# Kernel optimization log

Measured on AMD Instinct MI355X. Metric: run time of the kernel, lower is better.

The kernel has to match this reference:

```python
import jax, jax.numpy as jnp
import numpy as np

B, NQ, NK = 4, 2048, 2048
DQ = DK = DV = 512
H = 8
DS = DV // H  # 64


def _layernorm(x, g, b, eps=1e-5):
    m = jnp.mean(x, axis=-1, keepdims=True)
    v = jnp.var(x, axis=-1, keepdims=True)
    return (x - m) * jax.lax.rsqrt(v + eps) * g + b


def setup_inputs() -> dict:
    key = jax.random.key(0)
    ks = jax.random.split(key, 16)
    def lin(k, fan_in, fan_out):
        # torch nn.Linear default init: U(-1/sqrt(fan_in), 1/sqrt(fan_in))
        bound = 1.0 / np.sqrt(fan_in)
        k1, k2 = jax.random.split(k)
        W = jax.random.uniform(k1, (fan_in, fan_out), jnp.float32, -bound, bound)
        b = jax.random.uniform(k2, (fan_out,), jnp.float32, -bound, bound)
        return W, b
    Wq, bq = lin(ks[0], DQ, DV)
    Wk, bk = lin(ks[1], DK, DV)
    Wv, bv = lin(ks[2], DK, DV)
    W0, b0 = lin(ks[3], DV, DV)
    W1, b1 = lin(ks[4], DV, DV)
    # xavier_uniform for kp/vp of shape (1, DS): bound = sqrt(6/(1+DS))
    xb = np.sqrt(6.0 / (1 + DS))
    kp = jax.random.uniform(ks[5], (DS,), jnp.float32, -xb, xb)
    vp = jax.random.uniform(ks[6], (DS,), jnp.float32, -xb, xb)
    return {
        "Q": jax.random.normal(ks[7], (B, NQ, DQ), jnp.float32),
        "K": jax.random.normal(ks[8], (B, NK, DK), jnp.float32),
        "Kpos": jax.random.uniform(ks[9], (B, NQ, NK), jnp.float32),
        "Wq": Wq, "bq": bq, "Wk": Wk, "bk": bk, "Wv": Wv, "bv": bv,
        "kp": kp, "vp": vp,
        "W0": W0, "b0": b0, "W1": W1, "b1": b1,
        "g0": jnp.ones((DV,), jnp.float32), "be0": jnp.zeros((DV,), jnp.float32),
        "g1": jnp.ones((DV,), jnp.float32), "be1": jnp.zeros((DV,), jnp.float32),
    }


def reference(Q, K, Kpos, Wq, bq, Wk, bk, Wv, bv, kp, vp, W0, b0, W1, b1, g0, be0, g1, be1):
    Qp = Q @ Wq + bq                       # [B,NQ,DV]
    Kp = K @ Wk + bk                       # [B,NK,DV]
    Vp = K @ Wv + bv                       # [B,NK,DV]
    # head split (torch split/cat along batch == reshape to [B,N,H,DS])
    Qh = Qp.reshape(B, NQ, H, DS)
    Kh = Kp.reshape(B, NK, H, DS)
    Vh = Vp.reshape(B, NK, H, DS)
    scale = 1.0 / np.sqrt(DV)              # NOTE: original scales by sqrt(dim_V), not per-head dim
    scores = jnp.einsum('bqhd,bkhd->bhqk', Qh, Kh) * scale
    # ShawRE key bias: KE[b,h,q,k] = Kpos[b,q,k] * <Qh[b,q,h,:], kp>
    qkp = jnp.einsum('bqhd,d->bhq', Qh, kp)          # [B,H,NQ]
    scores = scores + Kpos[:, None, :, :] * qkp[:, :, :, None]
    A = jax.nn.softmax(scores, axis=-1)              # [B,H,NQ,NK]
    out = jnp.einsum('bhqk,bkhd->bqhd', A, Vh)       # [B,NQ,H,DS]
    # ShawRE value bias: VE[b,q,h,:] = (sum_k A*Kpos) * vp
    akp = jnp.einsum('bhqk,bqk->bhq', A, Kpos)       # [B,H,NQ]
    out = out + akp.transpose(0, 2, 1)[..., None] * vp
    O = (Qh + out).reshape(B, NQ, DV)
    O = _layernorm(O, g0, be0)
    resO = O
    O = jax.nn.relu(O @ W0 + b0)           # fc_o[0] with relu (numlayers=2)
    O = resO + jax.nn.relu(O @ W1 + b1)    # fc_o[-1] + residual
    O = _layernorm(O, g1, be1)
    return O
```

## Files before the change

### kernel.cpp

```cpp
#include <hip/hip_runtime.h>
#include <math.h>

#define Bx  4
#define NQx 2048
#define NKx 2048
#define Dx  512
#define Hx  8

typedef __attribute__((ext_vector_type(8))) __bf16 bf16x8;
typedef __attribute__((ext_vector_type(4))) float f32x4;
typedef __attribute__((ext_vector_type(16))) float f32x16;

typedef const __attribute__((address_space(1))) unsigned int* gas_ptr;
typedef __attribute__((address_space(3))) unsigned int* lds_ptr;

__device__ __forceinline__ void gload16(const void* g, void* l){
  __builtin_amdgcn_global_load_lds((gas_ptr)g, (lds_ptr)l, 16, 0, 0);
}

__device__ __forceinline__ unsigned short f2bf(float f){
  union { float f; unsigned int u; } v; v.f = f;
  unsigned int r = (v.u + 0x7FFFu + ((v.u >> 16) & 1u)) >> 16;
  return (unsigned short)r;
}
__device__ __forceinline__ float bf2f(unsigned short u){
  union { unsigned int u; float f; } v; v.u = ((unsigned int)u) << 16; return v.f;
}
__device__ __forceinline__ unsigned int cvtpk_bf16(float a, float b){
  unsigned int d;
  asm("v_cvt_pk_bf16_f32 %0, %1, %2" : "=v"(d) : "v"(a), "v"(b));
  return d;
}
__device__ __forceinline__ void plane32_swap(unsigned int& a, unsigned int& b){
  asm("v_permlane32_swap_b32 %0, %1" : "+v"(a), "+v"(b));
}

__global__ __launch_bounds__(256) void mab_cvt(
    const float* __restrict__ S0, unsigned short* __restrict__ D0,
    const float* __restrict__ S1, unsigned short* __restrict__ D1, int n4each)
{
  int total = n4each*2;
  for (int i = blockIdx.x*blockDim.x + threadIdx.x; i < total; i += gridDim.x*blockDim.x){
    const float* S; unsigned short* D; int j;
    if (i < n4each){ S = S0; D = D0; j = i; } else { S = S1; D = D1; j = i - n4each; }
    float4 v = ((const float4*)S)[j];
    ushort4 o; o.x=f2bf(v.x); o.y=f2bf(v.y); o.z=f2bf(v.z); o.w=f2bf(v.w);
    ((ushort4*)D)[j] = o;
  }
}

__global__ __launch_bounds__(256) void mab_wt(
    const float* __restrict__ Wq, const float* __restrict__ Wk, const float* __restrict__ Wv,
    const float* __restrict__ W0, const float* __restrict__ W1,
    unsigned short* __restrict__ Wt)
{
  __shared__ unsigned short T[64][72];
  const int z = blockIdx.z;
  const float* W = (z==0)?Wq:(z==1)?Wk:(z==2)?Wv:(z==3)?W0:W1;
  unsigned short* O = Wt + (size_t)z*512*512;
  const int k0 = blockIdx.x*64, n0 = blockIdx.y*64;
  const int tid = threadIdx.x;
  #pragma unroll
  for (int i=0;i<4;++i){
    int id = tid + i*256;
    int r = id>>4, c4 = id&15;
    float4 v = *(const float4*)(W + (size_t)(k0+r)*512 + n0 + c4*4);
    ushort4 o; o.x=f2bf(v.x); o.y=f2bf(v.y); o.z=f2bf(v.z); o.w=f2bf(v.w);
    *(ushort4*)&T[r][c4*4] = o;
  }
  __syncthreads();
  #pragma unroll
  for (int i=0;i<2;++i){
    int id = tid + i*256;
    int c = id>>3, r8 = id&7;
    union { unsigned short u[8]; uint4 v; } o;
    #pragma unroll
    for (int j=0;j<8;++j) o.u[j] = T[r8*8+j][c];
    *(uint4*)(O + (size_t)(n0+c)*512 + k0 + r8*8) = o.v;
  }
}

__global__ __launch_bounds__(256) void mab_vt(
    const unsigned short* __restrict__ Vp, unsigned short* __restrict__ Vpt)
{
  __shared__ unsigned short T[64][72];
  const int r0 = blockIdx.x*64;
  const int c0 = blockIdx.y*64;
  const int b  = blockIdx.z;
  const int tid = threadIdx.x;
  #pragma unroll
  for (int i=0;i<2;++i){
    int id = tid + i*256;
    int r = id>>3, c8 = id&7;
    *(uint4*)&T[r][c8*8] = *(const uint4*)(Vp + (size_t)(b*NKx + r0+r)*512 + c0 + c8*8);
  }
  __syncthreads();
  #pragma unroll
  for (int i=0;i<2;++i){
    int id = tid + i*256;
    int c = id>>3, r8 = id&7;
    union { unsigned short u[8]; uint4 v; } o;
    #pragma unroll
    for (int j=0;j<8;++j) o.u[j] = T[r8*8+j][c];
    *(uint4*)(Vpt + ((size_t)(b*512) + c0 + c)*NKx + r0 + r8*8) = o.v;
  }
}

__global__ __launch_bounds__(256) void mab_gemm_mfma(
    const unsigned short* __restrict__ A0, const unsigned short* __restrict__ A1,
    const unsigned short* __restrict__ Wt,
    const float* __restrict__ bias0, const float* __restrict__ bias1, const float* __restrict__ bias2,
    const float* __restrict__ res,
    unsigned short* __restrict__ Cb, float* __restrict__ Cf,
    int relu, float scaleArg, size_t zstride)
{
  __shared__ unsigned short As[128][64];
  __shared__ unsigned short Bs[128][64];
  const int z = blockIdx.z;
  const unsigned short* A = (z == 0) ? A0 : A1;
  const unsigned short* W = Wt + (size_t)z*512*512;
  const float* bias = (z==0)?bias0:((z==1)?bias1:bias2);
  const float sc = (z==1) ? scaleArg : 1.0f;
  const int m0 = blockIdx.y*128, n0 = blockIdx.x*128;
  const int tid = threadIdx.x, w = tid>>6, lane = tid&63, g = lane>>4, q16 = lane&15;
  const int wr = w>>1, wc = w&1;

  f32x4 acc[4][4];
  #pragma unroll
  for (int m=0;m<4;++m)
    #pragma unroll
    for (int n=0;n<4;++n) acc[m][n] = (f32x4){0.f,0.f,0.f,0.f};

  for (int k0 = 0; k0 < 512; k0 += 64){
    __syncthreads();
    #pragma unroll
    for (int i=0;i<4;++i){
      int o   = (w*4 + i)*1024 + lane*16;
      int row = o >> 7;
      int c   = (o >> 4) & 7;
      int cs  = c ^ (row & 7);
      gload16(A + (size_t)(m0+row)*512 + k0 + cs*8, (char*)&As[0][0] + (w*4+i)*1024);
      gload16(W + (size_t)(n0+row)*512 + k0 + cs*8, (char*)&Bs[0][0] + (w*4+i)*1024);
    }
    __syncthreads();
    #pragma unroll
    for (int ks=0;ks<2;++ks){
      bf16x8 af[4], bfr[4];
      #pragma unroll
      for (int m=0;m<4;++m){
        int row = wr*64 + m*16 + q16;
        int c   = (ks*4 + g) ^ (row & 7);
        af[m] = *(const bf16x8*)((const char*)&As[0][0] + row*128 + c*16);
      }
      #pragma unroll
      for (int n=0;n<4;++n){
        int row = wc*64 + n*16 + q16;
        int c   = (ks*4 + g) ^ (row & 7);
        bfr[n] = *(const bf16x8*)((const char*)&Bs[0][0] + row*128 + c*16);
      }
      #pragma unroll
      for (int m=0;m<4;++m)
        #pragma unroll
        for (int n=0;n<4;++n)
          acc[m][n] = __builtin_amdgcn_mfma_f32_16x16x32_bf16(af[m], bfr[n], acc[m][n], 0,0,0);
    }
  }

  #pragma unroll
  for (int m=0;m<4;++m){
    const int rowl = wr*64 + m*16 + g*4;
    #pragma unroll
    for (int n=0;n<4;++n){
      const int col = n0 + wc*64 + n*16 + q16;
      const float bv = bias[col];
      #pragma unroll
      for (int r=0;r<4;++r){
        float v = acc[m][n][r] + bv;
        if (relu) v = fmaxf(v, 0.f);
        v *= sc;
        size_t off = (size_t)(m0 + rowl + r)*512 + col;
        if (res) v += res[off];
        if (Cb) Cb[(size_t)z*zstride + off] = f2bf(v);
        if (Cf) Cf[off] = v;
      }
    }
  }
}

__global__ __launch_bounds__(256) void mab_attn2(
    const unsigned short* __restrict__ Qp, const unsigned short* __restrict__ Kp,
    const unsigned short* __restrict__ Vpt,
    const float* __restrict__ Kpos, const float* __restrict__ kp, const float* __restrict__ vp,
    float* __restrict__ X)
{
  __shared__ unsigned short Kb[2][64][64];
  __shared__ unsigned short Vb[2][64][64];
  __shared__ unsigned short Qs[128][72];

  const int q0 = blockIdx.x*128;
  const int h  = blockIdx.y;
  const int b  = blockIdx.z;
  const int tid = threadIdx.x, w = tid>>6, lane = tid&63;
  const int q32 = lane & 31, hi = lane >> 5;

  const unsigned short* Qg = Qp + ((size_t)(b*NQx + q0))*Dx + h*64;
  const unsigned short* Kg = Kp + ((size_t)b*NKx)*Dx + h*64;
  const unsigned short* Vg = Vpt + ((size_t)(b*512) + h*64)*NKx;
  const float* KProw = Kpos + (size_t)b*NQx*NKx + (size_t)(q0 + w*32 + q32)*NKx;

  const int sr = lane>>3;
  const int sc = lane&7;

  #pragma unroll
  for (int i=0;i<2;++i){
    int r  = i*8 + sr;
    int cs = sc ^ (r & 7);
    gload16(Kg + (size_t)(w*16 + r)*Dx + cs*8, (char*)&Kb[0][0][0] + w*2048 + i*1024);
    gload16(Vg + (size_t)(w*16 + r)*NKx + cs*8, (char*)&Vb[0][0][0] + w*2048 + i*1024);
  }
  #pragma unroll
  for (int i=0;i<4;++i){
    int id = tid + i*256;
    int r = id>>3, c8 = id&7;
    *(uint4*)&Qs[r][c8*8] = *(const uint4*)(Qg + (size_t)r*Dx + c8*8);
  }
  __syncthreads();

  bf16x8 qf[4];
  #pragma unroll
  for (int ds=0; ds<4; ++ds)
    qf[ds] = *(const bf16x8*)&Qs[w*32 + q32][ds*16 + hi*8];

  float qkp = 0.f;
  #pragma unroll
  for (int ds=0; ds<4; ++ds){
    union { bf16x8 v; unsigned short u[8]; } qa; qa.v = qf[ds];
    #pragma unroll
    for (int j=0;j<8;++j)
      qkp = fmaf(bf2f(qa.u[j]), kp[ds*16 + hi*8 + j], qkp);
  }
  qkp += __shfl_xor(qkp, 32);

  float m_i = -1e30f, l_i = 0.f, a_i = 0.f;
  f32x16 accT[2];
  #pragma unroll
  for (int db=0; db<2; ++db)
    #pragma unroll
    for (int r=0;r<16;++r) accT[db][r] = 0.f;

  const int NT = NKx/64;
  for (int kt = 0; kt < NT; ++kt){
    const int cur = kt & 1;
    const int k0 = kt*64;

    f32x4 kq[2][4];
    #pragma unroll
    for (int n=0;n<2;++n)
      #pragma unroll
      for (int a=0;a<4;++a)
        kq[n][a] = *(const f32x4*)(KProw + k0 + n*32 + a*8 + hi*4);
    __builtin_amdgcn_sched_barrier(0);

    if (kt+1 < NT){
      #pragma unroll
      for (int i=0;i<2;++i){
        int r  = i*8 + sr;
        int cs = sc ^ (r & 7);
        gload16(Kg + (size_t)(k0+64 + w*16 + r)*Dx + cs*8,
                (char*)&Kb[cur^1][0][0] + w*2048 + i*1024);
        gload16(Vg + (size_t)(w*16 + r)*NKx + (k0+64) + cs*8,
                (char*)&Vb[cur^1][0][0] + w*2048 + i*1024);
      }
    }
    __builtin_amdgcn_sched_barrier(0);

    f32x16 sT[2];
    __builtin_amdgcn_s_setprio(1);
    #pragma unroll
    for (int n=0;n<2;++n){
      f32x16 c;
      #pragma unroll
      for (int r=0;r<16;++r) c[r] = 0.f;
      #pragma unroll
      for (int ds=0; ds<4; ++ds){
        int row = n*32 + q32;
        int cc  = (ds*2 + hi) ^ (q32 & 7);
        bf16x8 kf = *(const bf16x8*)((const char*)&Kb[cur][0][0] + row*128 + cc*16);
        c = __builtin_amdgcn_mfma_f32_32x32x16_bf16(kf, qf[ds], c, 0,0,0);
      }
      sT[n] = c;
    }
    __builtin_amdgcn_s_setprio(0);

    #pragma unroll
    for (int n=0;n<2;++n)
      #pragma unroll
      for (int r=0;r<16;++r)
        sT[n][r] = fmaf(kq[n][r>>2][r&3], qkp, sT[n][r]);

    float rm = sT[0][0];
    #pragma unroll
    for (int r=1;r<16;++r) rm = fmaxf(rm, sT[0][r]);
    #pragma unroll
    for (int r=0;r<16;++r) rm = fmaxf(rm, sT[1][r]);
    rm = fmaxf(rm, __shfl_xor(rm, 32));

    if (!__all(rm <= m_i + 8.f)){
      float mnew = fmaxf(m_i, rm);
      float al = __expf(m_i - mnew);
      m_i = mnew;
      l_i *= al; a_i *= al;
      #pragma unroll
      for (int db=0; db<2; ++db)
        #pragma unroll
        for (int r=0;r<16;++r) accT[db][r] *= al;
    }

    float ps = 0.f, pk = 0.f;
    #pragma unroll
    for (int n=0;n<2;++n)
      #pragma unroll
      for (int r=0;r<16;++r){
        float p = __expf(sT[n][r] - m_i);
        sT[n][r] = p;
        ps += p;
        pk = fmaf(p, kq[n][r>>2][r&3], pk);
      }
    ps += __shfl_xor(ps, 32);
    pk += __shfl_xor(pk, 32);
    l_i += ps; a_i += pk;

    union PW { unsigned int u[4]; bf16x8 v; } pa[4];
    #pragma unroll
    for (int n=0;n<2;++n){
      unsigned int w0 = cvtpk_bf16(sT[n][0],  sT[n][1]);
      unsigned int w1 = cvtpk_bf16(sT[n][2],  sT[n][3]);
      unsigned int w2 = cvtpk_bf16(sT[n][4],  sT[n][5]);
      unsigned int w3 = cvtpk_bf16(sT[n][6],  sT[n][7]);
      unsigned int w4 = cvtpk_bf16(sT[n][8],  sT[n][9]);
      unsigned int w5 = cvtpk_bf16(sT[n][10], sT[n][11]);
      unsigned int w6 = cvtpk_bf16(sT[n][12], sT[n][13]);
      unsigned int w7 = cvtpk_bf16(sT[n][14], sT[n][15]);
      plane32_swap(w0, w2);
      plane32_swap(w1, w3);
      plane32_swap(w4, w6);
      plane32_swap(w5, w7);
      pa[n*2+0].u[0]=w0; pa[n*2+0].u[1]=w1; pa[n*2+0].u[2]=w2; pa[n*2+0].u[3]=w3;
      pa[n*2+1].u[0]=w4; pa[n*2+1].u[1]=w5; pa[n*2+1].u[2]=w6; pa[n*2+1].u[3]=w7;
    }

    __builtin_amdgcn_s_setprio(1);
    #pragma unroll
    for (int st=0; st<4; ++st){
      #pragma unroll
      for (int db=0; db<2; ++db){
        int row = db*32 + q32;
        int cc  = (st*2 + hi) ^ (q32 & 7);
        bf16x8 vf = *(const bf16x8*)((const char*)&Vb[cur][0][0] + row*128 + cc*16);
        accT[db] = __builtin_amdgcn_mfma_f32_32x32x16_bf16(vf, pa[st].v, accT[db], 0,0,0);
      }
    }
    __builtin_amdgcn_s_setprio(0);

    __syncthreads();
  }

  float inv = 1.0f / l_i;
  float aw  = a_i * inv;
  float* Xrow = X + ((size_t)(b*NQx + q0 + w*32 + q32))*Dx + h*64;
  #pragma unroll
  for (int db=0; db<2; ++db){
    #pragma unroll
    for (int a=0; a<4; ++a){
      int d0 = db*32 + a*8 + hi*4;
      f32x4 vpv = *(const f32x4*)(vp + d0);
      float4 o;
      o.x = fmaf(accT[db][a*4+0], inv, bf2f(Qs[w*32+q32][d0+0]) + aw*vpv[0]);
      o.y = fmaf(accT[db][a*4+1], inv, bf2f(Qs[w*32+q32][d0+1]) + aw*vpv[1]);
      o.z = fmaf(accT[db][a*4+2], inv, bf2f(Qs[w*32+q32][d0+2]) + aw*vpv[2]);
      o.w = fmaf(accT[db][a*4+3], inv, bf2f(Qs[w*32+q32][d0+3]) + aw*vpv[3]);
      *(float4*)(Xrow + d0) = o;
    }
  }
}

__global__ __launch_bounds__(256) void mab_ln2(
    const float* __restrict__ Xin, const float* __restrict__ g,
    const float* __restrict__ be, float* __restrict__ Yf, unsigned short* __restrict__ Yb)
{
  const int row = blockIdx.x;
  const int tid = threadIdx.x;
  const float* x = Xin + (size_t)row*Dx;
  float2 v = *(const float2*)(x + tid*2);
  float s  = v.x + v.y;
  float sq = fmaf(v.x,v.x, v.y*v.y);
  #pragma unroll
  for (int m=1; m<64; m<<=1){ s += __shfl_xor(s,m); sq += __shfl_xor(sq,m); }
  __shared__ float red[2][4];
  const int wid = tid>>6, lane = tid&63;
  if (lane==0){ red[0][wid]=s; red[1][wid]=sq; }
  __syncthreads();
  s  = red[0][0]+red[0][1]+red[0][2]+red[0][3];
  sq = red[1][0]+red[1][1]+red[1][2]+red[1][3];
  float mean = s*(1.0f/Dx);
  float var  = sq*(1.0f/Dx) - mean*mean;
  float rstd = rsqrtf(var + 1e-5f);
  float2 gg = *(const float2*)(g  + tid*2);
  float2 bb = *(const float2*)(be + tid*2);
  float2 o;
  o.x = (v.x-mean)*rstd*gg.x + bb.x;
  o.y = (v.y-mean)*rstd*gg.y + bb.y;
  if (Yf) *(float2*)(Yf + (size_t)row*Dx + tid*2) = o;
  if (Yb){
    ushort2 ob; ob.x = f2bf(o.x); ob.y = f2bf(o.y);
    *(ushort2*)(Yb + (size_t)row*Dx + tid*2) = ob;
  }
}

extern "C" void kernel_launch(void* const* d_in, const int* in_sizes, int n_in,
                              void* d_out, int out_size, void* d_ws, size_t ws_size,
                              hipStream_t stream)
{
  const float* Q    = (const float*)d_in[0];
  const float* K    = (const float*)d_in[1];
  const float* Kpos = (const float*)d_in[2];
  const float* Wq   = (const float*)d_in[3];
  const float* bq   = (const float*)d_in[4];
  const float* Wk   = (const float*)d_in[5];
  const float* bk   = (const float*)d_in[6];
  const float* Wv   = (const float*)d_in[7];
  const float* bv   = (const float*)d_in[8];
  const float* kp   = (const float*)d_in[9];
  const float* vp   = (const float*)d_in[10];
  const float* W0   = (const float*)d_in[11];
  const float* b0   = (const float*)d_in[12];
  const float* W1   = (const float*)d_in[13];
  const float* b1   = (const float*)d_in[14];
  const float* g0   = (const float*)d_in[15];
  const float* be0  = (const float*)d_in[16];
  const float* g1   = (const float*)d_in[17];
  const float* be1  = (const float*)d_in[18];
  float* out = (float*)d_out;
  char* wsb  = (char*)d_ws;

  const size_t MB = 1024*1024;
  unsigned short* Qp  = (unsigned short*)(wsb);
  unsigned short* Kp  = (unsigned short*)(wsb + 8*MB);
  unsigned short* Vp  = (unsigned short*)(wsb + 16*MB);
  float*          O0  = (float*)         (wsb + 24*MB);
  unsigned short* Qb  = (unsigned short*)(wsb + 40*MB);
  unsigned short* Kb  = (unsigned short*)(wsb + 48*MB);
  unsigned short* Wt  = (unsigned short*)(wsb + 56*MB);
  unsigned short* Vpt = Qb;
  unsigned short* O0b = Kb;
  unsigned short* T1  = Vp;

  const float scale = 0.044194173824159216f;
  const size_t ZS = (size_t)8192*512;

  mab_cvt<<<2048, 256, 0, stream>>>(Q, Qb, K, Kb, (8192*512)/4);
  mab_wt<<<dim3(8,8,5), 256, 0, stream>>>(Wq, Wk, Wv, W0, W1, Wt);
  mab_gemm_mfma<<<dim3(4,64,3), 256, 0, stream>>>(
      Qb, Kb, Wt, bq, bk, bv, nullptr, Qp, nullptr, 0, scale, ZS);
  mab_vt<<<dim3(32,8,4), 256, 0, stream>>>(Vp, Vpt);
  mab_attn2<<<dim3(16,8,4), 256, 0, stream>>>(Qp, Kp, Vpt, Kpos, kp, vp, out);
  mab_ln2<<<8192, 256, 0, stream>>>(out, g0, be0, O0, O0b);
  mab_gemm_mfma<<<dim3(4,64,1), 256, 0, stream>>>(
      O0b, nullptr, Wt + (size_t)3*512*512, b0, b0, b0, nullptr, T1, nullptr, 1, 1.0f, 0);
  mab_gemm_mfma<<<dim3(4,64,1), 256, 0, stream>>>(
      T1, nullptr, Wt + (size_t)4*512*512, b1, b1, b1, O0, nullptr, out, 1, 1.0f, 0);
  mab_ln2<<<8192, 256, 0, stream>>>(out, g1, be1, out, nullptr);
}
```

Baseline: 204.2 us.

## Fuse fp32-to-bf16 conversion into projection GEMM and tune attention softmax loop

Drops the separate Q/K conversion kernel. A new projection GEMM reads fp32 Q/K directly, register-prefetches the next A tile and packs it to bf16 in LDS. In attention, the Kpos tile loads are software-pipelined one tile ahead through a ping-pong of register arrays. The softmax switches to base-2 exponent by folding log2(e) into the K scale and qkp, uses max3 reductions, and raises the lazy-rescale threshold to match. This removes a kernel launch and a full fp32->bf16 round trip through memory, and hides Kpos latency, at the cost of more registers in attention.

```diff
diff --git a/kernel.cpp b/kernel.cpp
--- a/kernel.cpp
+++ b/kernel.cpp
@@ -34,19 +34,11 @@
 __device__ __forceinline__ void plane32_swap(unsigned int& a, unsigned int& b){
   asm("v_permlane32_swap_b32 %0, %1" : "+v"(a), "+v"(b));
 }
-
-__global__ __launch_bounds__(256) void mab_cvt(
-    const float* __restrict__ S0, unsigned short* __restrict__ D0,
-    const float* __restrict__ S1, unsigned short* __restrict__ D1, int n4each)
-{
-  int total = n4each*2;
-  for (int i = blockIdx.x*blockDim.x + threadIdx.x; i < total; i += gridDim.x*blockDim.x){
-    const float* S; unsigned short* D; int j;
-    if (i < n4each){ S = S0; D = D0; j = i; } else { S = S1; D = D1; j = i - n4each; }
-    float4 v = ((const float4*)S)[j];
-    ushort4 o; o.x=f2bf(v.x); o.y=f2bf(v.y); o.z=f2bf(v.z); o.w=f2bf(v.w);
-    ((ushort4*)D)[j] = o;
-  }
+__device__ __forceinline__ float fexp2(float x){
+  float d; asm("v_exp_f32 %0, %1" : "=v"(d) : "v"(x)); return d;
+}
+__device__ __forceinline__ float fmax3(float a, float b, float c){
+  float d; asm("v_max3_f32 %0, %1, %2, %3" : "=v"(d) : "v"(a), "v"(b), "v"(c)); return d;
 }
 
 __global__ __launch_bounds__(256) void mab_wt(
@@ -106,21 +98,110 @@
   }
 }
 
-__global__ __launch_bounds__(256) void mab_gemm_mfma(
-    const unsigned short* __restrict__ A0, const unsigned short* __restrict__ A1,
+__global__ __launch_bounds__(256) void mab_gemm_proj(
+    const float* __restrict__ Qf, const float* __restrict__ Kf,
     const unsigned short* __restrict__ Wt,
-    const float* __restrict__ bias0, const float* __restrict__ bias1, const float* __restrict__ bias2,
-    const float* __restrict__ res,
-    unsigned short* __restrict__ Cb, float* __restrict__ Cf,
-    int relu, float scaleArg, size_t zstride)
+    const float* __restrict__ bq, const float* __restrict__ bk, const float* __restrict__ bv,
+    unsigned short* __restrict__ Cb, float kscale)
 {
   __shared__ unsigned short As[128][64];
   __shared__ unsigned short Bs[128][64];
   const int z = blockIdx.z;
-  const unsigned short* A = (z == 0) ? A0 : A1;
+  const float* A = (z==0) ? Qf : Kf;
   const unsigned short* W = Wt + (size_t)z*512*512;
-  const float* bias = (z==0)?bias0:((z==1)?bias1:bias2);
-  const float sc = (z==1) ? scaleArg : 1.0f;
+  const float* bias = (z==0)?bq:((z==1)?bk:bv);
+  const float sc = (z==1) ? kscale : 1.0f;
+  const int m0 = blockIdx.y*128, n0 = blockIdx.x*128;
+  const int tid = threadIdx.x, w = tid>>6, lane = tid&63, g = lane>>4, q16 = lane&15;
+  const int wr = w>>1, wc = w&1;
+
+  f32x4 acc[4][4];
+  #pragma unroll
+  for (int m=0;m<4;++m)
+    #pragma unroll
+    for (int n=0;n<4;++n) acc[m][n] = (f32x4){0.f,0.f,0.f,0.f};
+
+  float4 areg[8];
+  #pragma unroll
+  for (int i=0;i<8;++i){
+    int id = i*256 + tid, row = id>>4, qc = id&15;
+    areg[i] = *(const float4*)(A + (size_t)(m0+row)*512 + qc*4);
+  }
+
+  for (int k0 = 0; k0 < 512; k0 += 64){
+    __syncthreads();
+    #pragma unroll
+    for (int i=0;i<8;++i){
+      int id = i*256 + tid, row = id>>4, qc = id&15;
+      unsigned int lo = cvtpk_bf16(areg[i].x, areg[i].y);
+      unsigned int hi = cvtpk_bf16(areg[i].z, areg[i].w);
+      unsigned int* dst = (unsigned int*)((char*)&As[0][0] + row*128
+                          + ((qc>>1) ^ (row&7))*16 + (qc&1)*8);
+      dst[0] = lo; dst[1] = hi;
+    }
+    #pragma unroll
+    for (int i=0;i<4;++i){
+      int o   = (w*4 + i)*1024 + lane*16;
+      int row = o >> 7;
+      int c   = (o >> 4) & 7;
+      int cs  = c ^ (row & 7);
+      gload16(W + (size_t)(n0+row)*512 + k0 + cs*8, (char*)&Bs[0][0] + (w*4+i)*1024);
+    }
+    __syncthreads();
+    if (k0 + 64 < 512){
+      #pragma unroll
+      for (int i=0;i<8;++i){
+        int id = i*256 + tid, row = id>>4, qc = id&15;
+        areg[i] = *(const float4*)(A + (size_t)(m0+row)*512 + (k0+64) + qc*4);
+      }
+    }
+    #pragma unroll
+    for (int ks=0;ks<2;++ks){
+      bf16x8 af[4], bfr[4];
+      #pragma unroll
+      for (int m=0;m<4;++m){
+        int row = wr*64 + m*16 + q16;
+        int c   = (ks*4 + g) ^ (row & 7);
+        af[m] = *(const bf16x8*)((const char*)&As[0][0] + row*128 + c*16);
+      }
+      #pragma unroll
+      for (int n=0;n<4;++n){
+        int row = wc*64 + n*16 + q16;
+        int c   = (ks*4 + g) ^ (row & 7);
+        bfr[n] = *(const bf16x8*)((const char*)&Bs[0][0] + row*128 + c*16);
+      }
+      #pragma unroll
+      for (int m=0;m<4;++m)
+        #pragma unroll
+        for (int n=0;n<4;++n)
+          acc[m][n] = __builtin_amdgcn_mfma_f32_16x16x32_bf16(af[m], bfr[n], acc[m][n], 0,0,0);
+    }
+  }
+
+  const size_t ZS = (size_t)8192*512;
+  #pragma unroll
+  for (int m=0;m<4;++m){
+    const int rowl = wr*64 + m*16 + g*4;
+    #pragma unroll
+    for (int n=0;n<4;++n){
+      const int col = n0 + wc*64 + n*16 + q16;
+      const float bv2 = bias[col];
+      #pragma unroll
+      for (int r=0;r<4;++r){
+        float v = (acc[m][n][r] + bv2) * sc;
+        Cb[(size_t)z*ZS + (size_t)(m0 + rowl + r)*512 + col] = f2bf(v);
+      }
+    }
+  }
+}
+
+__global__ __launch_bounds__(256) void mab_gemm_mfma(
+    const unsigned short* __restrict__ A, const unsigned short* __restrict__ W,
+    const float* __restrict__ bias, const float* __restrict__ res,
+    unsigned short* __restrict__ Cb, float* __restrict__ Cf, int relu)
+{
+  __shared__ unsigned short As[128][64];
+  __shared__ unsigned short Bs[128][64];
   const int m0 = blockIdx.y*128, n0 = blockIdx.x*128;
   const int tid = threadIdx.x, w = tid>>6, lane = tid&63, g = lane>>4, q16 = lane&15;
   const int wr = w>>1, wc = w&1;
@@ -177,10 +258,9 @@
       for (int r=0;r<4;++r){
         float v = acc[m][n][r] + bv;
         if (relu) v = fmaxf(v, 0.f);
-        v *= sc;
         size_t off = (size_t)(m0 + rowl + r)*512 + col;
         if (res) v += res[off];
-        if (Cb) Cb[(size_t)z*zstride + off] = f2bf(v);
+        if (Cb) Cb[off] = f2bf(v);
         if (Cf) Cf[off] = v;
       }
     }
@@ -218,6 +298,12 @@
     gload16(Kg + (size_t)(w*16 + r)*Dx + cs*8, (char*)&Kb[0][0][0] + w*2048 + i*1024);
     gload16(Vg + (size_t)(w*16 + r)*NKx + cs*8, (char*)&Vb[0][0][0] + w*2048 + i*1024);
   }
+  f32x4 kqA[2][4], kqB[2][4];
+  #pragma unroll
+  for (int n=0;n<2;++n)
+    #pragma unroll
+    for (int a=0;a<4;++a)
+      kqA[n][a] = *(const f32x4*)(KProw + n*32 + a*8 + hi*4);
   #pragma unroll
   for (int i=0;i<4;++i){
     int id = tid + i*256;
@@ -240,6 +326,7 @@
       qkp = fmaf(bf2f(qa.u[j]), kp[ds*16 + hi*8 + j], qkp);
   }
   qkp += __shfl_xor(qkp, 32);
+  qkp *= 1.4426950408889634f;
 
   float m_i = -1e30f, l_i = 0.f, a_i = 0.f;
   f32x16 accT[2];
@@ -249,26 +336,24 @@
     for (int r=0;r<16;++r) accT[db][r] = 0.f;
 
   const int NT = NKx/64;
-  for (int kt = 0; kt < NT; ++kt){
+
+  auto tile_body = [&](int kt, f32x4 (&kqc)[2][4], f32x4 (&kqn)[2][4]) {
     const int cur = kt & 1;
     const int k0 = kt*64;
-
-    f32x4 kq[2][4];
-    #pragma unroll
-    for (int n=0;n<2;++n)
-      #pragma unroll
-      for (int a=0;a<4;++a)
-        kq[n][a] = *(const f32x4*)(KProw + k0 + n*32 + a*8 + hi*4);
-    __builtin_amdgcn_sched_barrier(0);
-
     if (kt+1 < NT){
+      const int k1 = k0 + 64;
+      #pragma unroll
+      for (int n=0;n<2;++n)
+        #pragma unroll
+        for (int a=0;a<4;++a)
+          kqn[n][a] = *(const f32x4*)(KProw + k1 + n*32 + a*8 + hi*4);
       #pragma unroll
       for (int i=0;i<2;++i){
         int r  = i*8 + sr;
         int cs = sc ^ (r & 7);
-        gload16(Kg + (size_t)(k0+64 + w*16 + r)*Dx + cs*8,
+        gload16(Kg + (size_t)(k1 + w*16 + r)*Dx + cs*8,
                 (char*)&Kb[cur^1][0][0] + w*2048 + i*1024);
-        gload16(Vg + (size_t)(w*16 + r)*NKx + (k0+64) + cs*8,
+        gload16(Vg + (size_t)(w*16 + r)*NKx + k1 + cs*8,
                 (char*)&Vb[cur^1][0][0] + w*2048 + i*1024);
       }
     }
@@ -296,19 +381,25 @@
     for (int n=0;n<2;++n)
       #pragma unroll
       for (int r=0;r<16;++r)
-        sT[n][r] = fmaf(kq[n][r>>2][r&3], qkp, sT[n][r]);
-
-    float rm = sT[0][0];
-    #pragma unroll
-    for (int r=1;r<16;++r) rm = fmaxf(rm, sT[0][r]);
-    #pragma unroll
-    for (int r=0;r<16;++r) rm = fmaxf(rm, sT[1][r]);
+        sT[n][r] = fmaf(kqc[n][r>>2][r&3], qkp, sT[n][r]);
+
+    float m0a = fmax3(sT[0][0], sT[0][1], sT[0][2]);
+    float m0b = fmax3(sT[0][3], sT[0][4], sT[0][5]);
+    float m0c = fmax3(sT[0][6], sT[0][7], sT[0][8]);
+    float m0d = fmax3(sT[0][9], sT[0][10], sT[0][11]);
+    float m0e = fmax3(sT[0][12], sT[0][13], sT[0][14]);
+    float m1a = fmax3(sT[1][0], sT[1][1], sT[1][2]);
+    float m1b = fmax3(sT[1][3], sT[1][4], sT[1][5]);
+    float m1c = fmax3(sT[1][6], sT[1][7], sT[1][8]);
+    float m1d = fmax3(sT[1][9], sT[1][10], sT[1][11]);
+    float m1e = fmax3(sT[1][12], sT[1][13], sT[1][14]);
+    float rm = fmax3(fmax3(m0a, m0b, m0c), fmax3(m0d, m0e, sT[0][15]),
+                     fmax3(fmax3(m1a, m1b, m1c), fmax3(m1d, m1e, sT[1][15]), m_i));
     rm = fmaxf(rm, __shfl_xor(rm, 32));
 
-    if (!__all(rm <= m_i + 8.f)){
-      float mnew = fmaxf(m_i, rm);
-      float al = __expf(m_i - mnew);
-      m_i = mnew;
+    if (!__all(rm <= m_i + 11.544f)){
+      float al = fexp2(m_i - rm);
+      m_i = rm;
       l_i *= al; a_i *= al;
       #pragma unroll
       for (int db=0; db<2; ++db)
@@ -321,10 +412,10 @@
     for (int n=0;n<2;++n)
       #pragma unroll
       for (int r=0;r<16;++r){
-        float p = __expf(sT[n][r] - m_i);
+        float p = fexp2(sT[n][r] - m_i);
         sT[n][r] = p;
         ps += p;
-        pk = fmaf(p, kq[n][r>>2][r&3], pk);
+        pk = fmaf(p, kqc[n][r>>2][r&3], pk);
       }
     ps += __shfl_xor(ps, 32);
     pk += __shfl_xor(pk, 32);
@@ -363,6 +454,11 @@
     __builtin_amdgcn_s_setprio(0);
 
     __syncthreads();
+  };
+
+  for (int kt = 0; kt < NT; kt += 2){
+    tile_body(kt,   kqA, kqB);
+    tile_body(kt+1, kqB, kqA);
   }
 
   float inv = 1.0f / l_i;
@@ -448,26 +544,21 @@
   unsigned short* Kp  = (unsigned short*)(wsb + 8*MB);
   unsigned short* Vp  = (unsigned short*)(wsb + 16*MB);
   float*          O0  = (float*)         (wsb + 24*MB);
-  unsigned short* Qb  = (unsigned short*)(wsb + 40*MB);
-  unsigned short* Kb  = (unsigned short*)(wsb + 48*MB);
+  unsigned short* Vpt = (unsigned short*)(wsb + 40*MB);
+  unsigned short* O0b = (unsigned short*)(wsb + 48*MB);
   unsigned short* Wt  = (unsigned short*)(wsb + 56*MB);
-  unsigned short* Vpt = Qb;
-  unsigned short* O0b = Kb;
   unsigned short* T1  = Vp;
 
-  const float scale = 0.044194173824159216f;
-  const size_t ZS = (size_t)8192*512;
-
-  mab_cvt<<<2048, 256, 0, stream>>>(Q, Qb, K, Kb, (8192*512)/4);
+  const float kscale = 0.044194173824159216f * 1.4426950408889634f;
+
   mab_wt<<<dim3(8,8,5), 256, 0, stream>>>(Wq, Wk, Wv, W0, W1, Wt);
-  mab_gemm_mfma<<<dim3(4,64,3), 256, 0, stream>>>(
-      Qb, Kb, Wt, bq, bk, bv, nullptr, Qp, nullptr, 0, scale, ZS);
+  mab_gemm_proj<<<dim3(4,64,3), 256, 0, stream>>>(Q, K, Wt, bq, bk, bv, Qp, kscale);
   mab_vt<<<dim3(32,8,4), 256, 0, stream>>>(Vp, Vpt);
   mab_attn2<<<dim3(16,8,4), 256, 0, stream>>>(Qp, Kp, Vpt, Kpos, kp, vp, out);
   mab_ln2<<<8192, 256, 0, stream>>>(out, g0, be0, O0, O0b);
   mab_gemm_mfma<<<dim3(4,64,1), 256, 0, stream>>>(
-      O0b, nullptr, Wt + (size_t)3*512*512, b0, b0, b0, nullptr, T1, nullptr, 1, 1.0f, 0);
+      O0b, Wt + (size_t)3*512*512, b0, nullptr, T1, nullptr, 1);
   mab_gemm_mfma<<<dim3(4,64,1), 256, 0, stream>>>(
-      T1, nullptr, Wt + (size_t)4*512*512, b1, b1, b1, O0, nullptr, out, 1, 1.0f, 0);
+      T1, Wt + (size_t)4*512*512, b1, O0, nullptr, out, 1);
   mab_ln2<<<8192, 256, 0, stream>>>(out, g1, be1, out, nullptr);
 }
```

New measurement: 244.6 us. 1.2x slower.
